# Kernel tuning notes

Measured on AMD Instinct MI355X. Metric: run time of the kernel, lower is better.

The kernel has to match this reference:

```python
import jax, jax.numpy as jnp
import numpy as np
from jax import lax

GAMMA = 2.0
BLANK = 0
NEG = -1e30  # log-space 'zero'
T, B, C, L = 1000, 64, 256, 100


def setup_inputs() -> dict:
    key = jax.random.key(0)
    k1, k2 = jax.random.split(key)
    # valid log-probabilities, as produced by a model's log_softmax head
    log_probs = jax.nn.log_softmax(jax.random.normal(k1, (T, B, C), dtype=jnp.float32), axis=-1)
    # concatenated targets, blank (0) excluded as CTC requires
    targets = jax.random.randint(k2, (B * L,), 1, C, dtype=jnp.int32)
    input_lengths = jnp.full((B,), T, dtype=jnp.int32)
    target_lengths = jnp.full((B,), L, dtype=jnp.int32)
    return {"log_probs": log_probs, "targets": targets,
            "input_lengths": input_lengths, "target_lengths": target_lengths}


def _ctc_loss(log_probs, targets2d, input_lengths, target_lengths):
    # log_probs: (T,B,C); targets2d: (B,L). Returns per-sample NLL (B,).
    Tt, Bb, _ = log_probs.shape
    Ll = targets2d.shape[1]
    S = 2 * Ll + 1  # extended label sequence: blank interleaved
    ext = jnp.full((Bb, S), BLANK, dtype=jnp.int32).at[:, 1::2].set(targets2d)
    # emission log-probs for each extended symbol: (T,B,S)
    emit = jnp.take_along_axis(log_probs, jnp.broadcast_to(ext[None], (Tt, Bb, S)), axis=2)
    # skip-transition allowed where symbol is non-blank and differs from s-2
    allow2 = jnp.concatenate(
        [jnp.zeros((Bb, 2), bool), (ext[:, 2:] != BLANK) & (ext[:, 2:] != ext[:, :-2])], axis=1)

    def shiftk(a, k):
        return jnp.pad(a, ((0, 0), (k, 0)), constant_values=NEG)[:, :S]

    alpha0 = jnp.full((Bb, S), NEG, jnp.float32).at[:, 0].set(emit[0, :, 0]).at[:, 1].set(emit[0, :, 1])

    def step(alpha, e):
        a1 = shiftk(alpha, 1)
        a2 = jnp.where(allow2, shiftk(alpha, 2), NEG)
        m = jnp.maximum(jnp.maximum(alpha, a1), a2)
        new = m + jnp.log(jnp.exp(alpha - m) + jnp.exp(a1 - m) + jnp.exp(a2 - m)) + e
        return new, new

    _, rest = lax.scan(step, alpha0, emit[1:])
    alphas = jnp.concatenate([alpha0[None], rest], axis=0)  # (T,B,S)
    b = jnp.arange(Bb)
    last = alphas[input_lengths - 1, b]  # (B,S) at each sample's final step
    ll = jnp.logaddexp(last[b, 2 * target_lengths], last[b, 2 * target_lengths - 1])
    # zero_infinity=True semantics
    return jnp.where(ll > NEG / 2, -ll, 0.0)


def reference(log_probs, targets, input_lengths, target_lengths):
    targets2d = targets.reshape(B, L)
    loss = _ctc_loss(log_probs, targets2d, input_lengths, target_lengths)  # (B,)
    # focal weights: mean-over-time prob of each target symbol (computed under no_grad in torch)
    mean_probs = jnp.exp(log_probs).mean(axis=0)  # (B,C)
    target_probs = lax.stop_gradient(
        jnp.take_along_axis(mean_probs, targets2d, axis=1).reshape(-1))  # (B*L,)
    focal_weight = (1.0 - target_probs) ** GAMMA
    # torch broadcasting quirk: (total,) * (B,1) -> (B,total); mean over all
    return (focal_weight[None, :] * loss[:, None]).mean()
```

## Files before the change

kernel.cpp:

```cpp
#include <hip/hip_runtime.h>
#include <cstdint>

#define T_DIM 1000
#define B_DIM 64
#define C_DIM 256
#define L_DIM 100
#define S_DIM (2 * L_DIM + 1)
#define CH 32
#define NPROD 7
#define RPW 5
#define MEAN_BLOCKS 256
#define MEAN_ROWS 125

#define DPP_I(x, ctrl) __builtin_amdgcn_update_dpp(0, (x), (ctrl), 0xF, 0xF, true)
#define DPP_F(x, ctrl) __int_as_float(DPP_I(__float_as_int(x), (ctrl)))

#define PIN(x) asm volatile("" : "+v"(x))

__device__ __forceinline__ float wave_max_dpp(float x) {
    x = fmaxf(x, DPP_F(x, 0x111));
    x = fmaxf(x, DPP_F(x, 0x112));
    x = fmaxf(x, DPP_F(x, 0x114));
    x = fmaxf(x, DPP_F(x, 0x118));
    x = fmaxf(x, DPP_F(x, 0x142));
    x = fmaxf(x, DPP_F(x, 0x143));
    return __int_as_float(__builtin_amdgcn_readlane(__float_as_int(x), 63));
}

__global__ __launch_bounds__(512, 1) void ctc_fused(
        const float* __restrict__ lp,
        const int* __restrict__ tgt,
        const int* __restrict__ il,
        const int* __restrict__ tl,
        float* __restrict__ ws_mean,
        float* __restrict__ ws_loss) {
    const int blk = blockIdx.x;
    const uint32_t rstride = B_DIM * C_DIM;

    if (blk >= B_DIM) {
        const int mb = blk - B_DIM;
        const int b = mb >> 2;
        const int half = threadIdx.x >> 8;
        const int c = threadIdx.x & 255;
        const int slice = ((mb & 3) << 1) + half;
        const float* p = lp + (size_t)b * C_DIM + c + (size_t)(slice * MEAN_ROWS) * rstride;
        float s0 = 0.f, s1 = 0.f, s2 = 0.f, s3 = 0.f, s4 = 0.f;
        for (int t = 0; t < MEAN_ROWS; t += 5) {
            s0 += __expf(p[(size_t)(t + 0) * rstride]);
            s1 += __expf(p[(size_t)(t + 1) * rstride]);
            s2 += __expf(p[(size_t)(t + 2) * rstride]);
            s3 += __expf(p[(size_t)(t + 3) * rstride]);
            s4 += __expf(p[(size_t)(t + 4) * rstride]);
        }
        atomicAdd(&ws_mean[b * C_DIM + c], (s0 + s1 + s2 + s3 + s4) * (1.0f / T_DIM));
        return;
    }

    __shared__ __align__(16) float rows[2][CH][C_DIM];

    const int tid = threadIdx.x;
    const int lane = tid & 63;
    const int wave = tid >> 6;
    const int b = blk;
    const int* trow = tgt + b * L_DIM;
    const int ilen = il[b];
    const int tlen = tl[b];

    const int i1 = 2 * lane;
    const int i3 = 2 * lane + 1;
    const int c1 = (i1 < L_DIM) ? trow[i1] : 0;
    const int c3 = (i3 < L_DIM) ? trow[i3] : 0;
    const int c1m = (i1 >= 1 && i1 - 1 < L_DIM) ? trow[i1 - 1] : -1;
    const float m1 = ((i1 >= 1) && (c1 != c1m)) ? 1.0f : 0.0f;
    const float m3 = (c3 != c1) ? 1.0f : 0.0f;

    const float f0 = (4 * lane + 0 < S_DIM) ? 1.0f : 0.0f;
    const float f1 = (4 * lane + 1 < S_DIM) ? 1.0f : 0.0f;
    const float f2 = (4 * lane + 2 < S_DIM) ? 1.0f : 0.0f;
    const float f3 = (4 * lane + 3 < S_DIM) ? 1.0f : 0.0f;

    const float* base = lp + (size_t)b * C_DIM;

    float a0 = 0.f, a1 = 0.f, a2 = 0.f, a3 = 0.f;
    {
        float i0 = __expf(base[0]);
        float i1v = __expf(base[c1]);
        if (lane == 0 && wave == 0) { a0 = i0; a1 = i1v; }
    }
    float ls = 0.f;

    auto produce = [&](int cc) {
        const int p = cc & 1;
        const int tstart = 1 + cc * CH;
        float4 v[RPW];
#pragma unroll
        for (int k = 0; k < RPW; ++k) {
            const int d = (wave - 1) + NPROD * k;
            if (d < CH) {
                int t = tstart + d; t = (t < ilen) ? t : (ilen - 1);
                v[k] = *(const float4*)(base + (size_t)t * rstride + (lane << 2));
            }
        }
#pragma unroll
        for (int k = 0; k < RPW; ++k) {
            const int d = (wave - 1) + NPROD * k;
            if (d < CH) { PIN(v[k].x); PIN(v[k].y); PIN(v[k].z); PIN(v[k].w); }
        }
#pragma unroll
        for (int k = 0; k < RPW; ++k) {
            const int d = (wave - 1) + NPROD * k;
            if (d < CH) {
                float4 e;
                e.x = __expf(v[k].x); e.y = __expf(v[k].y);
                e.z = __expf(v[k].z); e.w = __expf(v[k].w);
                *(float4*)&rows[p][d][lane << 2] = e;
            }
        }
    };

    auto step = [&](float pb, float p1e, float p3e) {
        const float p3 = DPP_F(a3, 0x138);
        const float a01 = a0 + a1;
        const float n0 = (a0 + p3) * pb;
        const float n1 = fmaf(m1, p3, a01) * p1e;
        const float n2 = (a2 + a1) * pb;
        const float n3 = (fmaf(m3, a1, a2) + a3) * p3e;
        a0 = n0; a1 = n1; a2 = n2; a3 = n3;
    };

#define RENORM() do {                                                       \
        a0 *= f0; a1 *= f1; a2 *= f2; a3 *= f3;                             \
        const float mx = wave_max_dpp(fmaxf(fmaxf(a0, a1), fmaxf(a2, a3))); \
        const float inv = __builtin_amdgcn_rcpf(mx);                        \
        ls -= __logf(inv);                                                  \
        a0 *= inv; a1 *= inv; a2 *= inv; a3 *= inv;                         \
    } while (0)

    auto consume = [&](int cc) {
        const int p = cc & 1;
        const int tstart = 1 + cc * CH;
        if (tstart + CH <= ilen) {
#pragma unroll
            for (int d = 0; d < CH; ++d) {
                step(rows[p][d][0], rows[p][d][c1], rows[p][d][c3]);
                if ((d & 7) == 7) RENORM();
            }
        } else {
#pragma unroll
            for (int d = 0; d < CH; ++d) {
                if (tstart + d < ilen) {
                    step(rows[p][d][0], rows[p][d][c1], rows[p][d][c3]);
                    if ((d & 7) == 7) RENORM();
                }
            }
        }
    };

    const int nchunks = (ilen - 1 + CH - 1) / CH;
    if (wave != 0) produce(0);
    __syncthreads();
    for (int c = 0; c < nchunks; ++c) {
        if (wave != 0) produce(c + 1);
        else consume(c);
        __syncthreads();
    }
#undef RENORM

    if (wave != 0) return;

    const int s_hi = 2 * tlen;
    const int s_lo = 2 * tlen - 1;
    const int slot_hi = s_hi & 3, lane_hi = min(s_hi >> 2, 63);
    const int slot_lo = s_lo & 3, lane_lo = min(s_lo >> 2, 63);
    float ch = (slot_hi == 0) ? a0 : (slot_hi == 1) ? a1 : (slot_hi == 2) ? a2 : a3;
    float cl = (slot_lo == 0) ? a0 : (slot_lo == 1) ? a1 : (slot_lo == 2) ? a2 : a3;
    const float vh = __shfl(ch, lane_hi, 64);
    const float vl = __shfl(cl, lane_lo, 64);
    if (lane == 0) {
        const float s = vh + vl;
        const float loss = (s > 0.f) ? -(__logf(s) + ls) : 0.0f;
        ws_loss[b] = loss;
    }
}

__global__ __launch_bounds__(256) void ctc_finalize(
        const float* __restrict__ ws_mean, const float* __restrict__ ws_loss,
        const int* __restrict__ tgt, float* __restrict__ out) {
    const int tid = threadIdx.x;
    float fsum = 0.f;
#pragma unroll
    for (int k = 0; k < (B_DIM * L_DIM) / 256; ++k) {
        const int j = tid + k * 256;
        const int b = j / L_DIM;
        const int c = tgt[j];
        const float p = ws_mean[b * C_DIM + c];
        const float w = 1.0f - p;
        fsum += w * w;
    }
    float lsum = (tid < B_DIM) ? ws_loss[tid] : 0.f;
#pragma unroll
    for (int off = 32; off > 0; off >>= 1) {
        fsum += __shfl_down(fsum, off, 64);
        lsum += __shfl_down(lsum, off, 64);
    }
    __shared__ float sf[4], sl[4];
    const int w = tid >> 6;
    if ((tid & 63) == 0) { sf[w] = fsum; sl[w] = lsum; }
    __syncthreads();
    if (tid == 0) {
        const float F = sf[0] + sf[1] + sf[2] + sf[3];
        const float Lo = sl[0] + sl[1] + sl[2] + sl[3];
        out[0] = (F / (float)(B_DIM * L_DIM)) * (Lo / (float)B_DIM);
    }
}

extern "C" void kernel_launch(void* const* d_in, const int* in_sizes, int n_in,
                              void* d_out, int out_size, void* d_ws, size_t ws_size,
                              hipStream_t stream) {
    const float* lp = (const float*)d_in[0];
    const int* tgt = (const int*)d_in[1];
    const int* il = (const int*)d_in[2];
    const int* tl = (const int*)d_in[3];
    float* ws_mean = (float*)d_ws;
    float* ws_loss = ws_mean + B_DIM * C_DIM;

    hipMemsetAsync(ws_mean, 0, B_DIM * C_DIM * sizeof(float), stream);
    ctc_fused<<<dim3(B_DIM + MEAN_BLOCKS), dim3(512), 0, stream>>>(
        lp, tgt, il, tl, ws_mean, ws_loss);
    ctc_finalize<<<dim3(1), dim3(256), 0, stream>>>(ws_mean, ws_loss, tgt, (float*)d_out);
}
```

Baseline: 138.2 us.

## Pre-gather per-lane emissions into compact LDS layout and prefetch two steps ahead

Producer waves now stage raw rows in a scratch buffer and gather only the target-indexed emission values into a compact per-lane layout, so they exponentiate about 129 values per row instead of 256. The consumer wave then reads conflict-free contiguous per-lane values, software-prefetched two time steps ahead, instead of issuing random-index LDS gathers on the serial critical path. This costs extra LDS capacity, an extra scratch write/read round trip in the producers, and more registers for the prefetch.

After: 143.1 us. 1.04x slower.

```diff
diff --git a/kernel.cpp b/kernel.cpp
--- a/kernel.cpp
+++ b/kernel.cpp
@@ -9,6 +9,7 @@
 #define CH 32
 #define NPROD 7
 #define RPW 5
+#define EMW 132
 #define MEAN_BLOCKS 256
 #define MEAN_ROWS 125
 
@@ -56,7 +57,8 @@
         return;
     }
 
-    __shared__ __align__(16) float rows[2][CH][C_DIM];
+    __shared__ __align__(16) float scratch[NPROD][RPW][C_DIM];
+    __shared__ __align__(16) float emit[2][CH][EMW];
 
     const int tid = threadIdx.x;
     const int lane = tid & 63;
@@ -92,10 +94,11 @@
     auto produce = [&](int cc) {
         const int p = cc & 1;
         const int tstart = 1 + cc * CH;
+        const int w = wave - 1;
         float4 v[RPW];
 #pragma unroll
         for (int k = 0; k < RPW; ++k) {
-            const int d = (wave - 1) + NPROD * k;
+            const int d = w + NPROD * k;
             if (d < CH) {
                 int t = tstart + d; t = (t < ilen) ? t : (ilen - 1);
                 v[k] = *(const float4*)(base + (size_t)t * rstride + (lane << 2));
@@ -103,17 +106,23 @@
         }
 #pragma unroll
         for (int k = 0; k < RPW; ++k) {
-            const int d = (wave - 1) + NPROD * k;
+            const int d = w + NPROD * k;
             if (d < CH) { PIN(v[k].x); PIN(v[k].y); PIN(v[k].z); PIN(v[k].w); }
         }
 #pragma unroll
         for (int k = 0; k < RPW; ++k) {
-            const int d = (wave - 1) + NPROD * k;
+            const int d = w + NPROD * k;
+            if (d < CH) *(float4*)&scratch[w][k][lane << 2] = v[k];
+        }
+#pragma unroll
+        for (int k = 0; k < RPW; ++k) {
+            const int d = w + NPROD * k;
             if (d < CH) {
-                float4 e;
-                e.x = __expf(v[k].x); e.y = __expf(v[k].y);
-                e.z = __expf(v[k].z); e.w = __expf(v[k].w);
-                *(float4*)&rows[p][d][lane << 2] = e;
+                const float g1 = scratch[w][k][c1];
+                const float g3 = scratch[w][k][c3];
+                emit[p][d][lane] = __expf(g1);
+                emit[p][d][64 + lane] = __expf(g3);
+                if (lane == 0) emit[p][d][128] = __expf(v[k].x);
             }
         }
     };
@@ -140,16 +149,26 @@
         const int p = cc & 1;
         const int tstart = 1 + cc * CH;
         if (tstart + CH <= ilen) {
+            float pbA = emit[p][0][128], q1A = emit[p][0][lane], q3A = emit[p][0][64 + lane];
+            float pbB = emit[p][1][128], q1B = emit[p][1][lane], q3B = emit[p][1][64 + lane];
 #pragma unroll
             for (int d = 0; d < CH; ++d) {
-                step(rows[p][d][0], rows[p][d][c1], rows[p][d][c3]);
+                float pbN, q1N, q3N;
+                if (d + 2 < CH) {
+                    pbN = emit[p][d + 2][128];
+                    q1N = emit[p][d + 2][lane];
+                    q3N = emit[p][d + 2][64 + lane];
+                }
+                step(pbA, q1A, q3A);
                 if ((d & 7) == 7) RENORM();
+                pbA = pbB; q1A = q1B; q3A = q3B;
+                if (d + 2 < CH) { pbB = pbN; q1B = q1N; q3B = q3N; }
             }
         } else {
 #pragma unroll
             for (int d = 0; d < CH; ++d) {
                 if (tstart + d < ilen) {
-                    step(rows[p][d][0], rows[p][d][c1], rows[p][d][c3]);
+                    step(emit[p][d][128], emit[p][d][lane], emit[p][d][64 + lane]);
                     if ((d & 7) == 7) RENORM();
                 }
             }
```
